# Kernel tuning notes

Hardware: AMD Instinct MI355X
Metric: run time of the kernel (lower is better)

Reference implementation:

```python
import jax, jax.numpy as jnp
import numpy as np


def setup_inputs() -> dict:
    key = jax.random.key(0)
    ks = jax.random.split(key, 7)
    T, B, I, H, O = 512, 64, 256, 512, 64
    std = 1.0 / np.sqrt(H)
    u = lambda k, shp: jax.random.uniform(k, shp, jnp.float32, -std, std)
    return {
        "x": jax.random.normal(ks[0], (T, B, I), jnp.float32),
        "x2h_w": u(ks[1], (3 * H, I)),
        "x2h_b": u(ks[2], (3 * H,)),
        "h2h_w": u(ks[3], (3 * H, H)),
        "h2h_b": u(ks[4], (3 * H,)),
        "fc_w": jax.random.normal(ks[5], (O, H), jnp.float32) * 0.05,
        "fc_b": jnp.zeros((O,), jnp.float32),
    }


def _gru_forward(x, x2h_w, x2h_b, h2h_w, h2h_b, fc_w, fc_b):
    T, B, _ = x.shape
    H = h2h_w.shape[1]
    # Precompute input projection for all timesteps: [T, B, 3H]
    x_proj = jnp.einsum("tbi,gi->tbg", x, x2h_w) + x2h_b

    def step(h, xp):
        h_t = h @ h2h_w.T + h2h_b  # [B, 3H]
        x_r, x_u, x_n = jnp.split(xp, 3, axis=1)
        h_r, h_u, h_n = jnp.split(h_t, 3, axis=1)
        reset = jax.nn.sigmoid(x_r + h_r)
        update = jax.nn.sigmoid(x_u + h_u)
        new = jnp.tanh(x_n + reset * h_n)
        hy = update * h + (1.0 - update) * new
        return hy, hy

    h0 = jnp.zeros((B, H), x.dtype)
    h_last, rnn_activity = jax.lax.scan(step, h0, x_proj)
    out = jnp.einsum("tbh,oh->tbo", rnn_activity, fc_w) + fc_b
    return out, rnn_activity


def reference(x, x2h_w, x2h_b, h2h_w, h2h_b, fc_w, fc_b):
    return _gru_forward(x, x2h_w, x2h_b, h2h_w, h2h_b, fc_w, fc_b)
```

## Files before the change

### kernel.cpp

```cpp
#include <hip/hip_runtime.h>
#include <cstdint>
#include <cstddef>

#define TT 512
#define BB 64
#define II 256
#define HH 512
#define GG 1536
#define OO 64
#define NWG 256
#define TAGPAD 16

__global__ __launch_bounds__(256)
void xproj_kernel(const float* __restrict__ x, const float* __restrict__ w,
                  const float* __restrict__ xb, float* __restrict__ xp)
{
    __shared__ float xs[64][68];
    __shared__ float ws[64][68];
    const int t  = blockIdx.y;
    const int g0 = blockIdx.x * 64;
    const int tid = threadIdx.x;
    const int gq = tid >> 4;
    const int bq = tid & 15;
    float acc[4][4];
#pragma unroll
    for (int j = 0; j < 4; ++j)
#pragma unroll
        for (int i = 0; i < 4; ++i) acc[j][i] = 0.f;

    for (int kc = 0; kc < 4; ++kc) {
        const int k0 = kc * 64;
        __syncthreads();
        for (int idx = tid; idx < 1024; idx += 256) {
            int r = idx >> 4, c4 = (idx & 15) * 4;
            float4 v = *(const float4*)(x + ((size_t)t * BB + r) * II + k0 + c4);
            xs[r][c4] = v.x; xs[r][c4+1] = v.y; xs[r][c4+2] = v.z; xs[r][c4+3] = v.w;
            float4 u = *(const float4*)(w + (size_t)(g0 + r) * II + k0 + c4);
            ws[r][c4] = u.x; ws[r][c4+1] = u.y; ws[r][c4+2] = u.z; ws[r][c4+3] = u.w;
        }
        __syncthreads();
#pragma unroll 4
        for (int k4 = 0; k4 < 16; ++k4) {
            float4 xv[4], wv[4];
#pragma unroll
            for (int i = 0; i < 4; ++i)
                xv[i] = *(const float4*)&xs[bq + 16*i][k4*4];
#pragma unroll
            for (int j = 0; j < 4; ++j)
                wv[j] = *(const float4*)&ws[gq + 16*j][k4*4];
#pragma unroll
            for (int j = 0; j < 4; ++j)
#pragma unroll
                for (int i = 0; i < 4; ++i) {
                    acc[j][i] = fmaf(wv[j].x, xv[i].x, acc[j][i]);
                    acc[j][i] = fmaf(wv[j].y, xv[i].y, acc[j][i]);
                    acc[j][i] = fmaf(wv[j].z, xv[i].z, acc[j][i]);
                    acc[j][i] = fmaf(wv[j].w, xv[i].w, acc[j][i]);
                }
        }
    }
#pragma unroll
    for (int j = 0; j < 4; ++j) {
        int g = g0 + gq + 16*j;
        float bg = xb[g];
#pragma unroll
        for (int i = 0; i < 4; ++i) {
            int b = bq + 16*i;
            xp[((size_t)t * GG + g) * BB + b] = acc[j][i] + bg;
        }
    }
}

__global__ __launch_bounds__(512, 2)
void scan_kernel(const float* __restrict__ xp, const float* __restrict__ hw,
                 const float* __restrict__ hbias, float* __restrict__ rnn,
                 int* __restrict__ tags)
{
    __shared__ float hlds[8][512];
    __shared__ float pad_[17408];
    __shared__ int s_rk;

    const int tid = threadIdx.x;
    ((volatile float*)pad_)[tid] = 0.f;

    int xcc;
    asm volatile("s_getreg_b32 %0, hwreg(HW_REG_XCC_ID)" : "=s"(xcc));
    const int g = xcc & 7;
    if (tid == 0) {
        __threadfence();
        s_rk = atomicAdd(tags + (size_t)g * 32 * TAGPAD + 8, 1);
    }
    __syncthreads();
    const int rk = s_rk;
    if (rk >= 32) return;

    const int w    = tid >> 6;
    const int l    = tid & 63;
    const int c0w  = rk * 16 + 2 * w;
    const int cc   = (l >> 3) & 1;
    const int col  = c0w + cc;
    const int ob   = 8 * g + (l & 7);

    const int sb = tid >> 6;
    const int sk = (tid & 63) * 8;

    float wreg[6][8];
#pragma unroll
    for (int rr = 0; rr < 6; ++rr) {
        const float* wp = hw + ((size_t)(rr >> 1) * HH + c0w + (rr & 1)) * HH;
        float4 a = *(const float4*)(wp + 4 * l);
        float4 b = *(const float4*)(wp + 256 + 4 * l);
        wreg[rr][0] = a.x; wreg[rr][1] = a.y; wreg[rr][2] = a.z; wreg[rr][3] = a.w;
        wreg[rr][4] = b.x; wreg[rr][5] = b.y; wreg[rr][6] = b.z; wreg[rr][7] = b.w;
    }
    const float bhr = hbias[col];
    const float bhu = hbias[HH + col];
    const float bhn = hbias[2 * HH + col];

    float hloc = 0.f;
    long long budget = 4000000;

    for (int t = 0; t < TT; ++t) {
        float xr = 0.f, xu = 0.f, xn = 0.f;
        if (l < 16) {
            const size_t xbase = (size_t)t * GG * BB;
            xr = xp[xbase + (size_t)(0 * HH + col) * BB + ob];
            xu = xp[xbase + (size_t)(1 * HH + col) * BB + ob];
            xn = xp[xbase + (size_t)(2 * HH + col) * BB + ob];
        }

        float g0v = 0.f, g1v = 0.f, g2v = 0.f;
        if (t > 0) {
            if (tid < 32) {
                const int* tp = tags + ((size_t)g * 32 + tid) * TAGPAD;
                int v;
                do {
                    asm volatile("global_load_dword %0, %1, off sc0 sc1\n\t"
                                 "s_waitcnt vmcnt(0)"
                                 : "=v"(v) : "v"(tp) : "memory");
                    if (v >= t) break;
                    __builtin_amdgcn_s_sleep(1);
                } while (--budget > 0);
            }
            __syncthreads();

            {
                const float* src = rnn + (size_t)(t - 1) * BB * HH
                                       + (size_t)(8 * g + sb) * HH + sk;
                float4 v0 = *(const float4*)src;
                float4 v1 = *(const float4*)(src + 4);
                *(float4*)&hlds[sb][sk]     = v0;
                *(float4*)&hlds[sb][sk + 4] = v1;
            }
            __syncthreads();

            float acc[8][6];
#pragma unroll
            for (int bi = 0; bi < 8; ++bi) {
                float4 hA = *(const float4*)&hlds[bi][4 * l];
                float4 hB = *(const float4*)&hlds[bi][256 + 4 * l];
#pragma unroll
                for (int rr = 0; rr < 6; ++rr) {
                    float a;
                    a = hA.x * wreg[rr][0];
                    a = fmaf(hA.y, wreg[rr][1], a);
                    a = fmaf(hA.z, wreg[rr][2], a);
                    a = fmaf(hA.w, wreg[rr][3], a);
                    a = fmaf(hB.x, wreg[rr][4], a);
                    a = fmaf(hB.y, wreg[rr][5], a);
                    a = fmaf(hB.z, wreg[rr][6], a);
                    a = fmaf(hB.w, wreg[rr][7], a);
                    acc[bi][rr] = a;
                }
            }

            const int s0 = l & 1, s1 = (l >> 1) & 1, s2 = (l >> 2) & 1;
            const int s3 = (l >> 3) & 1;
            float a1[4][6];
#pragma unroll
            for (int rr = 0; rr < 6; ++rr)
#pragma unroll
                for (int p = 0; p < 4; ++p) {
                    float lo = acc[2*p][rr], hi = acc[2*p+1][rr];
                    float send = s0 ? lo : hi;
                    float keep = s0 ? hi : lo;
                    a1[p][rr] = keep + __shfl_xor(send, 1, 64);
                }
            float a2[2][6];
#pragma unroll
            for (int rr = 0; rr < 6; ++rr)
#pragma unroll
                for (int p = 0; p < 2; ++p) {
                    float lo = a1[2*p][rr], hi = a1[2*p+1][rr];
                    float send = s1 ? lo : hi;
                    float keep = s1 ? hi : lo;
                    a2[p][rr] = keep + __shfl_xor(send, 2, 64);
                }
            float a3[6];
#pragma unroll
            for (int rr = 0; rr < 6; ++rr) {
                float lo = a2[0][rr], hi = a2[1][rr];
                float send = s2 ? lo : hi;
                float keep = s2 ? hi : lo;
                a3[rr] = keep + __shfl_xor(send, 4, 64);
            }
#pragma unroll
            for (int gate = 0; gate < 3; ++gate) {
                float lo = a3[2*gate], hi = a3[2*gate + 1];
                float send = s3 ? lo : hi;
                float keep = s3 ? hi : lo;
                float gv = keep + __shfl_xor(send, 8, 64);
                if (gate == 0) g0v = gv; else if (gate == 1) g1v = gv; else g2v = gv;
            }
            g0v += __shfl_xor(g0v, 16, 64); g0v += __shfl_xor(g0v, 32, 64);
            g1v += __shfl_xor(g1v, 16, 64); g1v += __shfl_xor(g1v, 32, 64);
            g2v += __shfl_xor(g2v, 16, 64); g2v += __shfl_xor(g2v, 32, 64);
        }

        if (l < 16) {
            float rg = 1.f / (1.f + __expf(-(xr + g0v + bhr)));
            float ug = 1.f / (1.f + __expf(-(xu + g1v + bhu)));
            float npre = xn + rg * (g2v + bhn);
            float e  = __expf(-2.f * npre);
            float nv = 2.f / (1.f + e) - 1.f;
            float hy = ug * hloc + (1.f - ug) * nv;
            hloc = hy;
            float* dst = rnn + ((size_t)t * BB + ob) * HH + col;
            asm volatile("global_store_dword %0, %1, off"
                         :: "v"(dst), "v"(hy) : "memory");
        }
        asm volatile("s_waitcnt vmcnt(0)" ::: "memory");
        __syncthreads();
        if (tid == 0) {
            int tv = t + 1;
            int* tp = tags + ((size_t)g * 32 + rk) * TAGPAD;
            asm volatile("global_store_dword %0, %1, off sc0 sc1"
                         :: "v"(tp), "v"(tv) : "memory");
        }
    }
}

__global__ __launch_bounds__(256)
void fc_kernel(const float* __restrict__ rnn, const float* __restrict__ fcw,
               const float* __restrict__ fcb, float* __restrict__ out)
{
    __shared__ float wlds[128][65];
    const int t = blockIdx.x;
    const int tid = threadIdx.x;
    const int o  = tid & 63;
    const int bg = tid >> 6;
    float acc[16];
#pragma unroll
    for (int i = 0; i < 16; ++i) acc[i] = 0.f;

    for (int kc = 0; kc < 4; ++kc) {
        const int k0 = kc * 128;
        __syncthreads();
        for (int idx = tid; idx < 64 * 32; idx += 256) {
            int oo = idx >> 5, kq = (idx & 31) * 4;
            float4 v = *(const float4*)(fcw + (size_t)oo * HH + k0 + kq);
            wlds[kq][oo] = v.x; wlds[kq+1][oo] = v.y;
            wlds[kq+2][oo] = v.z; wlds[kq+3][oo] = v.w;
        }
        __syncthreads();
#pragma unroll 2
        for (int k4 = 0; k4 < 32; ++k4) {
            float w0 = wlds[k4*4+0][o], w1 = wlds[k4*4+1][o];
            float w2 = wlds[k4*4+2][o], w3 = wlds[k4*4+3][o];
#pragma unroll
            for (int i = 0; i < 16; ++i) {
                int bb = bg * 16 + i;
                float4 h4 = *(const float4*)(rnn + ((size_t)t * BB + bb) * HH + k0 + k4*4);
                acc[i] = fmaf(h4.x, w0, fmaf(h4.y, w1, fmaf(h4.z, w2, fmaf(h4.w, w3, acc[i]))));
            }
        }
    }
    float bo = fcb[o];
#pragma unroll
    for (int i = 0; i < 16; ++i) {
        int bb = bg * 16 + i;
        out[((size_t)t * BB + bb) * OO + o] = acc[i] + bo;
    }
}

extern "C" void kernel_launch(void* const* d_in, const int* in_sizes, int n_in,
                              void* d_out, int out_size, void* d_ws, size_t ws_size,
                              hipStream_t stream)
{
    const float* x     = (const float*)d_in[0];
    const float* x2h_w = (const float*)d_in[1];
    const float* x2h_b = (const float*)d_in[2];
    const float* h2h_w = (const float*)d_in[3];
    const float* h2h_b = (const float*)d_in[4];
    const float* fc_w  = (const float*)d_in[5];
    const float* fc_b  = (const float*)d_in[6];

    float* out = (float*)d_out;
    float* rnn = (float*)d_out + (size_t)TT * BB * OO;

    float* xp = (float*)d_ws;
    const size_t xp_bytes = (size_t)TT * GG * BB * sizeof(float);
    int* tags = (int*)((char*)d_ws + xp_bytes);

    hipMemsetAsync(tags, 0, NWG * TAGPAD * sizeof(int), stream);

    dim3 gA(GG / 64, TT);
    xproj_kernel<<<gA, 256, 0, stream>>>(x, x2h_w, x2h_b, xp);
    scan_kernel<<<NWG, 512, 0, stream>>>(xp, h2h_w, h2h_b, rnn, tags);
    fc_kernel<<<TT, 256, 0, stream>>>(rnn, fc_w, fc_b, out);
}
```

Baseline: 2.557 ms.

## Split scan batch rows across two waves per column pair with 1024-thread blocks

The recurrent scan kernel doubles its workgroup to 1024 threads, so each pair of waves now shares a column pair and each wave handles 4 of the 8 batch rows. Per-wave FMA work and the shuffle-reduction depth are halved, and each thread copies one float4 of the previous hidden state into LDS instead of two. This shortens the serial per-timestep critical path, at the cost of more waves per CU, heavier block-wide barriers, and a tighter register budget under the new launch bounds.

Measured after the change: 2.494 ms. -2.4%, faster.

```diff
diff --git a/kernel.cpp b/kernel.cpp
--- a/kernel.cpp
+++ b/kernel.cpp
@@ -71,7 +71,7 @@
     }
 }
 
-__global__ __launch_bounds__(512, 2)
+__global__ __launch_bounds__(1024, 4)
 void scan_kernel(const float* __restrict__ xp, const float* __restrict__ hw,
                  const float* __restrict__ hbias, float* __restrict__ rnn,
                  int* __restrict__ tags)
@@ -96,13 +96,14 @@
 
     const int w    = tid >> 6;
     const int l    = tid & 63;
-    const int c0w  = rk * 16 + 2 * w;
-    const int cc   = (l >> 3) & 1;
-    const int col  = c0w + cc;
-    const int ob   = 8 * g + (l & 7);
-
-    const int sb = tid >> 6;
-    const int sk = (tid & 63) * 8;
+    const int cp   = w >> 1;
+    const int bh   = w & 1;
+    const int c0w  = rk * 16 + 2 * cp;
+    const int col  = c0w + ((l >> 2) & 1);
+    const int ob   = 8 * g + 4 * bh + (l & 3);
+
+    const int sb = tid >> 7;
+    const int sk = (tid & 127) * 4;
 
     float wreg[6][8];
 #pragma unroll
@@ -122,7 +123,7 @@
 
     for (int t = 0; t < TT; ++t) {
         float xr = 0.f, xu = 0.f, xn = 0.f;
-        if (l < 16) {
+        if (l < 8) {
             const size_t xbase = (size_t)t * GG * BB;
             xr = xp[xbase + (size_t)(0 * HH + col) * BB + ob];
             xu = xp[xbase + (size_t)(1 * HH + col) * BB + ob];
@@ -147,18 +148,15 @@
             {
                 const float* src = rnn + (size_t)(t - 1) * BB * HH
                                        + (size_t)(8 * g + sb) * HH + sk;
-                float4 v0 = *(const float4*)src;
-                float4 v1 = *(const float4*)(src + 4);
-                *(float4*)&hlds[sb][sk]     = v0;
-                *(float4*)&hlds[sb][sk + 4] = v1;
+                *(float4*)&hlds[sb][sk] = *(const float4*)src;
             }
             __syncthreads();
 
-            float acc[8][6];
-#pragma unroll
-            for (int bi = 0; bi < 8; ++bi) {
-                float4 hA = *(const float4*)&hlds[bi][4 * l];
-                float4 hB = *(const float4*)&hlds[bi][256 + 4 * l];
+            float acc[4][6];
+#pragma unroll
+            for (int bi = 0; bi < 4; ++bi) {
+                float4 hA = *(const float4*)&hlds[4 * bh + bi][4 * l];
+                float4 hB = *(const float4*)&hlds[4 * bh + bi][256 + 4 * l];
 #pragma unroll
                 for (int rr = 0; rr < 6; ++rr) {
                     float a;
@@ -175,49 +173,39 @@
             }
 
             const int s0 = l & 1, s1 = (l >> 1) & 1, s2 = (l >> 2) & 1;
-            const int s3 = (l >> 3) & 1;
-            float a1[4][6];
+            float a1[2][6];
 #pragma unroll
             for (int rr = 0; rr < 6; ++rr)
 #pragma unroll
-                for (int p = 0; p < 4; ++p) {
+                for (int p = 0; p < 2; ++p) {
                     float lo = acc[2*p][rr], hi = acc[2*p+1][rr];
                     float send = s0 ? lo : hi;
                     float keep = s0 ? hi : lo;
                     a1[p][rr] = keep + __shfl_xor(send, 1, 64);
                 }
-            float a2[2][6];
-#pragma unroll
-            for (int rr = 0; rr < 6; ++rr)
-#pragma unroll
-                for (int p = 0; p < 2; ++p) {
-                    float lo = a1[2*p][rr], hi = a1[2*p+1][rr];
-                    float send = s1 ? lo : hi;
-                    float keep = s1 ? hi : lo;
-                    a2[p][rr] = keep + __shfl_xor(send, 2, 64);
-                }
-            float a3[6];
+            float a2[6];
 #pragma unroll
             for (int rr = 0; rr < 6; ++rr) {
-                float lo = a2[0][rr], hi = a2[1][rr];
+                float lo = a1[0][rr], hi = a1[1][rr];
+                float send = s1 ? lo : hi;
+                float keep = s1 ? hi : lo;
+                a2[rr] = keep + __shfl_xor(send, 2, 64);
+            }
+            float a3[3];
+#pragma unroll
+            for (int gate = 0; gate < 3; ++gate) {
+                float lo = a2[2*gate], hi = a2[2*gate + 1];
                 float send = s2 ? lo : hi;
                 float keep = s2 ? hi : lo;
-                a3[rr] = keep + __shfl_xor(send, 4, 64);
-            }
-#pragma unroll
-            for (int gate = 0; gate < 3; ++gate) {
-                float lo = a3[2*gate], hi = a3[2*gate + 1];
-                float send = s3 ? lo : hi;
-                float keep = s3 ? hi : lo;
-                float gv = keep + __shfl_xor(send, 8, 64);
-                if (gate == 0) g0v = gv; else if (gate == 1) g1v = gv; else g2v = gv;
-            }
-            g0v += __shfl_xor(g0v, 16, 64); g0v += __shfl_xor(g0v, 32, 64);
-            g1v += __shfl_xor(g1v, 16, 64); g1v += __shfl_xor(g1v, 32, 64);
-            g2v += __shfl_xor(g2v, 16, 64); g2v += __shfl_xor(g2v, 32, 64);
-        }
-
-        if (l < 16) {
+                a3[gate] = keep + __shfl_xor(send, 4, 64);
+            }
+            g0v = a3[0]; g1v = a3[1]; g2v = a3[2];
+            g0v += __shfl_xor(g0v, 8, 64); g0v += __shfl_xor(g0v, 16, 64); g0v += __shfl_xor(g0v, 32, 64);
+            g1v += __shfl_xor(g1v, 8, 64); g1v += __shfl_xor(g1v, 16, 64); g1v += __shfl_xor(g1v, 32, 64);
+            g2v += __shfl_xor(g2v, 8, 64); g2v += __shfl_xor(g2v, 16, 64); g2v += __shfl_xor(g2v, 32, 64);
+        }
+
+        if (l < 8) {
             float rg = 1.f / (1.f + __expf(-(xr + g0v + bhr)));
             float ug = 1.f / (1.f + __expf(-(xu + g1v + bhu)));
             float npre = xn + rg * (g2v + bhn);
@@ -306,6 +294,6 @@
 
     dim3 gA(GG / 64, TT);
     xproj_kernel<<<gA, 256, 0, stream>>>(x, x2h_w, x2h_b, xp);
-    scan_kernel<<<NWG, 512, 0, stream>>>(xp, h2h_w, h2h_b, rnn, tags);
+    scan_kernel<<<NWG, 1024, 0, stream>>>(xp, h2h_w, h2h_b, rnn, tags);
     fc_kernel<<<TT, 256, 0, stream>>>(rnn, fc_w, fc_b, out);
 }
```
